# Kernel tuning notes

Measured on AMD Instinct MI355X. Metric: run time of the kernel, lower is better.

The kernel has to match this reference:

```python
import jax, jax.numpy as jnp
import numpy as np

VOXEL_SIZE = (0.2, 0.2)
GX, GY = 512, 512
MAX_PTS = 32  # max_points_per_pillar
IN_CH = 4


def setup_inputs() -> dict:
    key = jax.random.key(0)
    k1, k2 = jax.random.split(key)
    N, B = 400000, 2
    extent = GX * VOXEL_SIZE[0]  # 102.4 -> points land inside the grid
    all_points = jax.random.uniform(k1, (N, IN_CH), dtype=jnp.float32) * extent
    batch_indices = jnp.sort(jax.random.randint(k2, (N,), 0, B))
    return {"all_points": all_points, "batch_indices": batch_indices, "num_point_clouds": B}


def reference(all_points, batch_indices, num_point_clouds):
    B, P, C = num_point_clouds, MAX_PTS, all_points.shape[1]
    G = B * GX * GY  # total pillar slots
    vs = jnp.array(VOXEL_SIZE, dtype=all_points.dtype)
    # torch .long() truncates toward zero; points are non-negative here
    xy = (all_points[:, :2] / vs).astype(jnp.int32)
    xy = jnp.clip(xy, 0, jnp.array([GX - 1, GY - 1], dtype=jnp.int32))
    bidx = batch_indices.astype(jnp.int32)
    flat = bidx * (GX * GY) + xy[:, 0] * GY + xy[:, 1]  # [N]
    # counts per pillar (torch.unique + scatter_add equivalent)
    counts_full = jax.ops.segment_sum(jnp.ones_like(flat), flat, num_segments=G)
    occupied = counts_full > 0
    # torch.unique inverse index = rank of the pillar among occupied pillars
    inverse_full = jnp.cumsum(occupied.astype(jnp.int32)) - 1  # [G]
    inverse = inverse_full[flat]                               # [N]
    # drop ALL points of over-full pillars (count > P), as the original mask does
    mask = counts_full[flat] <= P
    pos = jnp.arange(flat.shape[0], dtype=jnp.int32)
    last_pos = jax.ops.segment_max(jnp.where(mask, pos, -1), inverse, num_segments=G)
    occ = last_pos >= 0
    winner = jnp.where(occ[:, None], all_points[jnp.clip(last_pos, 0)], 0.0)  # [G, C]
    # [M,C] assigned into [M,P,C] broadcasts over the P slot dim in torch
    voxel_features = jnp.broadcast_to(winner[:, None, :], (G, P, C)).reshape(B, GX, GY, P, C)
    # original allocates voxel_counts but never writes it
    voxel_counts = jnp.zeros((B, GX, GY), dtype=jnp.int32)
    return voxel_features, voxel_counts
```

## Files before the change

kernel.cpp:

```cpp
#include <hip/hip_runtime.h>

#define GXv 512
#define GYv 512
#define PMAX 32

constexpr int SCAN_TPB = 256;
constexpr int EPT = 8;
constexpr int EPB = SCAN_TPB * EPT;

__global__ void zero_int4_kernel(int4* __restrict__ p, int n4) {
    int i = blockIdx.x * blockDim.x + threadIdx.x;
    if (i < n4) p[i] = make_int4(0, 0, 0, 0);
}

__global__ void points_kernel(const float4* __restrict__ pts, const int* __restrict__ bidx,
                              int* __restrict__ counts, int* __restrict__ lastp, int N) {
    int i = blockIdx.x * blockDim.x + threadIdx.x;
    if (i >= N) return;
    float4 p = pts[i];
    int x = (int)(p.x / 0.2f);
    int y = (int)(p.y / 0.2f);
    x = min(max(x, 0), GXv - 1);
    y = min(max(y, 0), GYv - 1);
    int flat = bidx[i] * (GXv * GYv) + x * GYv + y;
    atomicAdd(&counts[flat], 1);
    atomicMax(&lastp[flat], i + 1);
}

__global__ void blocksum_kernel(const int* __restrict__ counts, int* __restrict__ blockSums, int G) {
    int t = threadIdx.x;
    int base = blockIdx.x * EPB + t * EPT;
    int s = 0;
#pragma unroll
    for (int k = 0; k < EPT; k++) {
        int g = base + k;
        if (g < G) s += (counts[g] > 0) ? 1 : 0;
    }
    __shared__ int sm[SCAN_TPB];
    sm[t] = s;
    __syncthreads();
    for (int off = SCAN_TPB / 2; off > 0; off >>= 1) {
        if (t < off) sm[t] += sm[t + off];
        __syncthreads();
    }
    if (t == 0) blockSums[blockIdx.x] = sm[0];
}

__global__ void scan_kernel(int* __restrict__ blockSums, int nb) {
    __shared__ int sm[1024];
    int t = threadIdx.x;
    int v = (t < nb) ? blockSums[t] : 0;
    sm[t] = v;
    __syncthreads();
    for (int off = 1; off < 1024; off <<= 1) {
        int add = (t >= off) ? sm[t - off] : 0;
        __syncthreads();
        sm[t] += add;
        __syncthreads();
    }
    if (t < nb) blockSums[t] = (t == 0) ? 0 : sm[t - 1];
}

__global__ void scatter_kernel(const int* __restrict__ counts, const int* __restrict__ lastp,
                               const int* __restrict__ blockOffsets, const float4* __restrict__ pts,
                               float4* __restrict__ compact, int G) {
    int t = threadIdx.x;
    int base = blockIdx.x * EPB + t * EPT;
    int cnt[EPT];
    int s = 0;
#pragma unroll
    for (int k = 0; k < EPT; k++) {
        int g = base + k;
        cnt[k] = (g < G) ? counts[g] : 0;
        s += (cnt[k] > 0) ? 1 : 0;
    }
    __shared__ int sm[SCAN_TPB];
    sm[t] = s;
    __syncthreads();
    for (int off = 1; off < SCAN_TPB; off <<= 1) {
        int add = (t >= off) ? sm[t - off] : 0;
        __syncthreads();
        sm[t] += add;
        __syncthreads();
    }
    int rank = blockOffsets[blockIdx.x] + ((t == 0) ? 0 : sm[t - 1]);
#pragma unroll
    for (int k = 0; k < EPT; k++) {
        int g = base + k;
        if (g < G && cnt[k] > 0) {
            if (cnt[k] <= PMAX) {
                int p = lastp[g] - 1;
                compact[rank] = pts[p];
            }
            rank++;
        }
    }
}

__global__ void broadcast_kernel(const float4* __restrict__ compact, float4* __restrict__ out4, int total4) {
    int i = blockIdx.x * blockDim.x + threadIdx.x;
    if (i < total4) out4[i] = compact[i >> 5];
}

extern "C" void kernel_launch(void* const* d_in, const int* in_sizes, int n_in,
                              void* d_out, int out_size, void* d_ws, size_t ws_size,
                              hipStream_t stream) {
    const float4* pts = (const float4*)d_in[0];
    const int* bidx = (const int*)d_in[1];
    int N = in_sizes[0] / 4;
    int G = out_size / 129;

    int* counts = (int*)d_ws;
    int* lastp = counts + G;
    float4* compact = (float4*)(lastp + G);
    int* blockSums = (int*)(compact + G);
    int nb = (G + EPB - 1) / EPB;

    int nz4 = (6 * G) / 4;
    zero_int4_kernel<<<(nz4 + 255) / 256, 256, 0, stream>>>((int4*)d_ws, nz4);

    points_kernel<<<(N + 255) / 256, 256, 0, stream>>>(pts, bidx, counts, lastp, N);
    blocksum_kernel<<<nb, SCAN_TPB, 0, stream>>>(counts, blockSums, G);
    scan_kernel<<<1, 1024, 0, stream>>>(blockSums, nb);
    scatter_kernel<<<nb, SCAN_TPB, 0, stream>>>(counts, lastp, blockSums, pts, compact, G);

    int total4 = G * PMAX;
    broadcast_kernel<<<(total4 + 255) / 256, 256, 0, stream>>>(compact, (float4*)d_out, total4);

    int nc4 = G / 4;
    zero_int4_kernel<<<(nc4 + 255) / 256, 256, 0, stream>>>(
        (int4*)((float*)d_out + (long)G * (PMAX * 4)), nc4);
}
```

Before: 327.6 us.

## Fuse all pillar-scatter stages into one cooperative kernel with grid syncs

```diff
diff --git a/kernel.cpp b/kernel.cpp
--- a/kernel.cpp
+++ b/kernel.cpp
@@ -1,105 +1,106 @@
 #include <hip/hip_runtime.h>
+#include <hip/hip_cooperative_groups.h>
+
+namespace cg = cooperative_groups;
 
 #define GXv 512
 #define GYv 512
 #define PMAX 32
 
-constexpr int SCAN_TPB = 256;
-constexpr int EPT = 8;
-constexpr int EPB = SCAN_TPB * EPT;
+constexpr int NB = 256;
+constexpr int NT = 512;
+constexpr int GT = NB * NT;
 
-__global__ void zero_int4_kernel(int4* __restrict__ p, int n4) {
-    int i = blockIdx.x * blockDim.x + threadIdx.x;
-    if (i < n4) p[i] = make_int4(0, 0, 0, 0);
-}
+typedef float vfloat4 __attribute__((ext_vector_type(4)));
+typedef int   vint4   __attribute__((ext_vector_type(4)));
 
-__global__ void points_kernel(const float4* __restrict__ pts, const int* __restrict__ bidx,
-                              int* __restrict__ counts, int* __restrict__ lastp, int N) {
-    int i = blockIdx.x * blockDim.x + threadIdx.x;
-    if (i >= N) return;
-    float4 p = pts[i];
-    int x = (int)(p.x / 0.2f);
-    int y = (int)(p.y / 0.2f);
-    x = min(max(x, 0), GXv - 1);
-    y = min(max(y, 0), GYv - 1);
-    int flat = bidx[i] * (GXv * GYv) + x * GYv + y;
-    atomicAdd(&counts[flat], 1);
-    atomicMax(&lastp[flat], i + 1);
-}
+__global__ void __launch_bounds__(NT) mega_kernel(
+        const float4* __restrict__ pts, const int* __restrict__ bidx,
+        int* __restrict__ counts, int* __restrict__ lastp,
+        float4* __restrict__ compact, int* __restrict__ agg,
+        float4* __restrict__ out4, int N, int G) {
+    cg::grid_group grid = cg::this_grid();
+    const int t = threadIdx.x;
+    const int b = blockIdx.x;
+    const int gtid = b * NT + t;
+    __shared__ int sm[NT];
 
-__global__ void blocksum_kernel(const int* __restrict__ counts, int* __restrict__ blockSums, int G) {
-    int t = threadIdx.x;
-    int base = blockIdx.x * EPB + t * EPT;
-    int s = 0;
-#pragma unroll
-    for (int k = 0; k < EPT; k++) {
-        int g = base + k;
-        if (g < G) s += (counts[g] > 0) ? 1 : 0;
+    {
+        vint4* z = (vint4*)counts;
+        int n4 = (6 * G) / 4;
+        vint4 zero4 = (vint4)0;
+        for (int i = gtid; i < n4; i += GT) z[i] = zero4;
     }
-    __shared__ int sm[SCAN_TPB];
+    grid.sync();
+
+    for (int i = gtid; i < N; i += GT) {
+        float4 p = pts[i];
+        int x = (int)(p.x / 0.2f);
+        int y = (int)(p.y / 0.2f);
+        x = min(max(x, 0), GXv - 1);
+        y = min(max(y, 0), GYv - 1);
+        int flat = bidx[i] * (GXv * GYv) + x * GYv + y;
+        atomicAdd(&counts[flat], 1);
+        atomicMax(&lastp[flat], i + 1);
+    }
+    grid.sync();
+
+    const int base = b * (NT * 4) + t * 4;
+    int4 c4 = *(const int4*)&counts[base];
+    int s = (c4.x > 0) + (c4.y > 0) + (c4.z > 0) + (c4.w > 0);
     sm[t] = s;
     __syncthreads();
-    for (int off = SCAN_TPB / 2; off > 0; off >>= 1) {
-        if (t < off) sm[t] += sm[t + off];
+    for (int off = 1; off < NT; off <<= 1) {
+        int v = (t >= off) ? sm[t - off] : 0;
+        __syncthreads();
+        sm[t] += v;
         __syncthreads();
     }
-    if (t == 0) blockSums[blockIdx.x] = sm[0];
-}
+    int excl = (t == 0) ? 0 : sm[t - 1];
+    if (t == 0) agg[b] = sm[NT - 1];
+    grid.sync();
 
-__global__ void scan_kernel(int* __restrict__ blockSums, int nb) {
-    __shared__ int sm[1024];
-    int t = threadIdx.x;
-    int v = (t < nb) ? blockSums[t] : 0;
-    sm[t] = v;
-    __syncthreads();
-    for (int off = 1; off < 1024; off <<= 1) {
-        int add = (t >= off) ? sm[t - off] : 0;
+    {
+        int av = (t < NB) ? agg[t] : 0;
+        sm[t] = av;
         __syncthreads();
-        sm[t] += add;
-        __syncthreads();
-    }
-    if (t < nb) blockSums[t] = (t == 0) ? 0 : sm[t - 1];
-}
-
-__global__ void scatter_kernel(const int* __restrict__ counts, const int* __restrict__ lastp,
-                               const int* __restrict__ blockOffsets, const float4* __restrict__ pts,
-                               float4* __restrict__ compact, int G) {
-    int t = threadIdx.x;
-    int base = blockIdx.x * EPB + t * EPT;
-    int cnt[EPT];
-    int s = 0;
+        for (int off = 1; off < NT; off <<= 1) {
+            int v = (t >= off) ? sm[t - off] : 0;
+            __syncthreads();
+            sm[t] += v;
+            __syncthreads();
+        }
+        int blockBase = (b == 0) ? 0 : sm[b - 1];
+        int rank = blockBase + excl;
+        int cnt[4] = {c4.x, c4.y, c4.z, c4.w};
 #pragma unroll
-    for (int k = 0; k < EPT; k++) {
-        int g = base + k;
-        cnt[k] = (g < G) ? counts[g] : 0;
-        s += (cnt[k] > 0) ? 1 : 0;
-    }
-    __shared__ int sm[SCAN_TPB];
-    sm[t] = s;
-    __syncthreads();
-    for (int off = 1; off < SCAN_TPB; off <<= 1) {
-        int add = (t >= off) ? sm[t - off] : 0;
-        __syncthreads();
-        sm[t] += add;
-        __syncthreads();
-    }
-    int rank = blockOffsets[blockIdx.x] + ((t == 0) ? 0 : sm[t - 1]);
-#pragma unroll
-    for (int k = 0; k < EPT; k++) {
-        int g = base + k;
-        if (g < G && cnt[k] > 0) {
-            if (cnt[k] <= PMAX) {
-                int p = lastp[g] - 1;
-                compact[rank] = pts[p];
+        for (int k = 0; k < 4; k++) {
+            if (cnt[k] > 0) {
+                if (cnt[k] <= PMAX) {
+                    int p = lastp[base + k] - 1;
+                    compact[rank] = pts[p];
+                }
+                rank++;
             }
-            rank++;
         }
     }
-}
+    grid.sync();
 
-__global__ void broadcast_kernel(const float4* __restrict__ compact, float4* __restrict__ out4, int total4) {
-    int i = blockIdx.x * blockDim.x + threadIdx.x;
-    if (i < total4) out4[i] = compact[i >> 5];
+    {
+        const int total4 = G * PMAX;
+        const vfloat4* csrc = (const vfloat4*)compact;
+        vfloat4* dst = (vfloat4*)out4;
+        for (int idx = gtid; idx < total4; idx += GT) {
+            vfloat4 v = csrc[idx >> 5];
+            __builtin_nontemporal_store(v, &dst[idx]);
+        }
+        vint4* outc4 = (vint4*)(out4 + (size_t)total4);
+        int nc4 = G / 4;
+        vint4 zero4 = (vint4)0;
+        for (int i = gtid; i < nc4; i += GT) {
+            __builtin_nontemporal_store(zero4, &outc4[i]);
+        }
+    }
 }
 
 extern "C" void kernel_launch(void* const* d_in, const int* in_sizes, int n_in,
@@ -113,21 +114,11 @@
     int* counts = (int*)d_ws;
     int* lastp = counts + G;
     float4* compact = (float4*)(lastp + G);
-    int* blockSums = (int*)(compact + G);
-    int nb = (G + EPB - 1) / EPB;
+    int* agg = (int*)(compact + G);
+    float4* out4 = (float4*)d_out;
 
-    int nz4 = (6 * G) / 4;
-    zero_int4_kernel<<<(nz4 + 255) / 256, 256, 0, stream>>>((int4*)d_ws, nz4);
-
-    points_kernel<<<(N + 255) / 256, 256, 0, stream>>>(pts, bidx, counts, lastp, N);
-    blocksum_kernel<<<nb, SCAN_TPB, 0, stream>>>(counts, blockSums, G);
-    scan_kernel<<<1, 1024, 0, stream>>>(blockSums, nb);
-    scatter_kernel<<<nb, SCAN_TPB, 0, stream>>>(counts, lastp, blockSums, pts, compact, G);
-
-    int total4 = G * PMAX;
-    broadcast_kernel<<<(total4 + 255) / 256, 256, 0, stream>>>(compact, (float4*)d_out, total4);
-
-    int nc4 = G / 4;
-    zero_int4_kernel<<<(nc4 + 255) / 256, 256, 0, stream>>>(
-        (int4*)((float*)d_out + (long)G * (PMAX * 4)), nc4);
+    void* args[] = {(void*)&pts, (void*)&bidx, (void*)&counts, (void*)&lastp,
+                    (void*)&compact, (void*)&agg, (void*)&out4, (void*)&N, (void*)&G};
+    (void)hipLaunchCooperativeKernel(reinterpret_cast<void*>(mega_kernel),
+                                     dim3(NB), dim3(NT), args, 0, stream);
 }
```

New measurement: 429.5 us. 31.1% more time.

## Fuse compaction scatter with broadcast and write output directly with nontemporal stores

Applied to the files above, without the earlier changes.

```diff
diff --git a/kernel.cpp b/kernel.cpp
--- a/kernel.cpp
+++ b/kernel.cpp
@@ -4,13 +4,15 @@
 #define GYv 512
 #define PMAX 32
 
-constexpr int SCAN_TPB = 256;
-constexpr int EPT = 8;
-constexpr int EPB = SCAN_TPB * EPT;
+typedef float vfloat4 __attribute__((ext_vector_type(4)));
+typedef int   vint4   __attribute__((ext_vector_type(4)));
 
-__global__ void zero_int4_kernel(int4* __restrict__ p, int n4) {
+__global__ void zero_kernel(vint4* __restrict__ ws, int na,
+                            vint4* __restrict__ outc, int nc) {
     int i = blockIdx.x * blockDim.x + threadIdx.x;
-    if (i < n4) p[i] = make_int4(0, 0, 0, 0);
+    vint4 z = (vint4)0;
+    if (i < na) ws[i] = z;
+    if (i < nc) outc[i] = z;
 }
 
 __global__ void points_kernel(const float4* __restrict__ pts, const int* __restrict__ bidx,
@@ -27,79 +29,84 @@
     atomicMax(&lastp[flat], i + 1);
 }
 
-__global__ void blocksum_kernel(const int* __restrict__ counts, int* __restrict__ blockSums, int G) {
-    int t = threadIdx.x;
-    int base = blockIdx.x * EPB + t * EPT;
-    int s = 0;
-#pragma unroll
-    for (int k = 0; k < EPT; k++) {
-        int g = base + k;
-        if (g < G) s += (counts[g] > 0) ? 1 : 0;
-    }
-    __shared__ int sm[SCAN_TPB];
-    sm[t] = s;
+__global__ void blocksum_kernel(const int* __restrict__ counts, int* __restrict__ bs) {
+    int t = threadIdx.x, b = blockIdx.x;
+    int2 c = ((const int2*)counts)[b * 256 + t];
+    __shared__ int sm[256];
+    sm[t] = (c.x > 0) + (c.y > 0);
     __syncthreads();
-    for (int off = SCAN_TPB / 2; off > 0; off >>= 1) {
+    for (int off = 128; off > 0; off >>= 1) {
         if (t < off) sm[t] += sm[t + off];
         __syncthreads();
     }
-    if (t == 0) blockSums[blockIdx.x] = sm[0];
+    if (t == 0) bs[b] = sm[0];
 }
 
-__global__ void scan_kernel(int* __restrict__ blockSums, int nb) {
+__global__ void scan_kernel(int* __restrict__ bs, int nb) {
     __shared__ int sm[1024];
     int t = threadIdx.x;
-    int v = (t < nb) ? blockSums[t] : 0;
+    int v = (t < nb) ? bs[t] : 0;
     sm[t] = v;
     __syncthreads();
     for (int off = 1; off < 1024; off <<= 1) {
-        int add = (t >= off) ? sm[t - off] : 0;
+        int a = (t >= off) ? sm[t - off] : 0;
         __syncthreads();
-        sm[t] += add;
+        sm[t] += a;
         __syncthreads();
     }
-    if (t < nb) blockSums[t] = (t == 0) ? 0 : sm[t - 1];
+    if (t < nb) bs[t] = (t == 0) ? 0 : sm[t - 1];
+    if (t == nb - 1) bs[nb] = sm[t];
 }
 
-__global__ void scatter_kernel(const int* __restrict__ counts, const int* __restrict__ lastp,
-                               const int* __restrict__ blockOffsets, const float4* __restrict__ pts,
-                               float4* __restrict__ compact, int G) {
-    int t = threadIdx.x;
-    int base = blockIdx.x * EPB + t * EPT;
-    int cnt[EPT];
-    int s = 0;
-#pragma unroll
-    for (int k = 0; k < EPT; k++) {
-        int g = base + k;
-        cnt[k] = (g < G) ? counts[g] : 0;
-        s += (cnt[k] > 0) ? 1 : 0;
-    }
-    __shared__ int sm[SCAN_TPB];
-    sm[t] = s;
+__global__ __launch_bounds__(256) void scatter_kernel(
+        const int* __restrict__ counts, const int* __restrict__ lastp,
+        const int* __restrict__ bs, const vfloat4* __restrict__ pts,
+        vfloat4* __restrict__ out, int G, int SB) {
+    int t = threadIdx.x, b = blockIdx.x;
+    int2 c2 = ((const int2*)counts)[b * 256 + t];
+    int2 lp2 = ((const int2*)lastp)[b * 256 + t];
+    int occ0 = (c2.x > 0), occ1 = (c2.y > 0);
+
+    __shared__ int sm[256];
+    __shared__ int enc[512];
+    __shared__ int lpl[512];
+    sm[t] = occ0 + occ1;
     __syncthreads();
-    for (int off = 1; off < SCAN_TPB; off <<= 1) {
-        int add = (t >= off) ? sm[t - off] : 0;
+    for (int off = 1; off < 256; off <<= 1) {
+        int a = (t >= off) ? sm[t - off] : 0;
         __syncthreads();
-        sm[t] += add;
+        sm[t] += a;
         __syncthreads();
     }
-    int rank = blockOffsets[blockIdx.x] + ((t == 0) ? 0 : sm[t - 1]);
-#pragma unroll
-    for (int k = 0; k < EPT; k++) {
-        int g = base + k;
-        if (g < G && cnt[k] > 0) {
-            if (cnt[k] <= PMAX) {
-                int p = lastp[g] - 1;
-                compact[rank] = pts[p];
-            }
-            rank++;
+    int excl = (t == 0) ? 0 : sm[t - 1];
+    int r0 = bs[b] + excl;
+    int r1 = r0 + occ0;
+    enc[2 * t]     = occ0 ? (r0 | ((c2.x > PMAX) ? (1 << 30) : 0)) : -1;
+    enc[2 * t + 1] = occ1 ? (r1 | ((c2.y > PMAX) ? (1 << 30) : 0)) : -1;
+    lpl[2 * t] = lp2.x;
+    lpl[2 * t + 1] = lp2.y;
+    __syncthreads();
+
+    int w = t >> 6, lane = t & 63, half = lane >> 5, slot = lane & 31;
+#pragma unroll 4
+    for (int it = 0; it < 64; it++) {
+        int cl = w * 128 + it * 2 + half;
+        int e = enc[cl];
+        if (e >= 0) {
+            int rank = e & 0x3FFFFFFF;
+            vfloat4 v = (vfloat4)0;
+            if (!(e & (1 << 30))) v = pts[lpl[cl] - 1];
+            __builtin_nontemporal_store(v, &out[(size_t)rank * 32 + slot]);
         }
     }
-}
 
-__global__ void broadcast_kernel(const float4* __restrict__ compact, float4* __restrict__ out4, int total4) {
-    int i = blockIdx.x * blockDim.x + threadIdx.x;
-    if (i < total4) out4[i] = compact[i >> 5];
+    int M = bs[SB];
+    size_t idx = (size_t)M * 32 + (size_t)b * 256 + t;
+    size_t end = (size_t)G * 32;
+    size_t stride = (size_t)SB * 256;
+    vfloat4 z = (vfloat4)0;
+    for (; idx < end; idx += stride)
+        __builtin_nontemporal_store(z, &out[idx]);
 }
 
 extern "C" void kernel_launch(void* const* d_in, const int* in_sizes, int n_in,
@@ -109,25 +116,19 @@
     const int* bidx = (const int*)d_in[1];
     int N = in_sizes[0] / 4;
     int G = out_size / 129;
+    int SB = G / 512;
 
     int* counts = (int*)d_ws;
     int* lastp = counts + G;
-    float4* compact = (float4*)(lastp + G);
-    int* blockSums = (int*)(compact + G);
-    int nb = (G + EPB - 1) / EPB;
+    int* bs = lastp + G;
+    vfloat4* out = (vfloat4*)d_out;
+    vint4* outc = (vint4*)((float*)d_out + (size_t)G * (PMAX * 4));
 
-    int nz4 = (6 * G) / 4;
-    zero_int4_kernel<<<(nz4 + 255) / 256, 256, 0, stream>>>((int4*)d_ws, nz4);
-
+    int na = (2 * G) / 4;
+    int nc = G / 4;
+    zero_kernel<<<(na + 255) / 256, 256, 0, stream>>>((vint4*)d_ws, na, outc, nc);
     points_kernel<<<(N + 255) / 256, 256, 0, stream>>>(pts, bidx, counts, lastp, N);
-    blocksum_kernel<<<nb, SCAN_TPB, 0, stream>>>(counts, blockSums, G);
-    scan_kernel<<<1, 1024, 0, stream>>>(blockSums, nb);
-    scatter_kernel<<<nb, SCAN_TPB, 0, stream>>>(counts, lastp, blockSums, pts, compact, G);
-
-    int total4 = G * PMAX;
-    broadcast_kernel<<<(total4 + 255) / 256, 256, 0, stream>>>(compact, (float4*)d_out, total4);
-
-    int nc4 = G / 4;
-    zero_int4_kernel<<<(nc4 + 255) / 256, 256, 0, stream>>>(
-        (int4*)((float*)d_out + (long)G * (PMAX * 4)), nc4);
+    blocksum_kernel<<<SB, 256, 0, stream>>>(counts, bs);
+    scan_kernel<<<1, 1024, 0, stream>>>(bs, SB);
+    scatter_kernel<<<SB, 256, 0, stream>>>(counts, lastp, bs, (const vfloat4*)pts, out, G, SB);
 }
```

New measurement: 318.6 us. 2.7% less time.
